# Optimization experiments

Measured on AMD Instinct MI355X. Metric: run time of the kernel, lower is better.

Reference implementation:

```python
import jax, jax.numpy as jnp
import numpy as np
from jax import lax

jax.config.update("jax_enable_x64", True)  # original torch code does the recurrence in float64

K_MAX = 32
L_MAX = 32
N = 65536


def setup_inputs() -> dict:
    key = jax.random.key(0)
    # strictly positive radii (r appears in a denominator)
    r = jax.random.uniform(key, (N,), dtype=jnp.float32, minval=0.1, maxval=10.0)
    return {"r": r}


def reference(r):
    # k = linspace(1, k_max, k_max)
    k = jnp.linspace(1.0, K_MAX, K_MAX, dtype=jnp.float64)          # [K]
    rk = r.astype(jnp.float64)[:, None] * k[None, :]                 # [N, K]

    lstart = L_MAX + int(np.sqrt(10 * L_MAX))                        # matches int(torch.sqrt(...))
    i_vals = jnp.arange(lstart, 0, -1, dtype=jnp.float64)            # lstart .. 1

    # downward (Miller) recurrence: j0 = (2i+1)/r * j1 - j2
    def step(carry, i):
        j1, j2 = carry
        j0 = (2.0 * i + 1.0) / rk * j1 - j2
        return (j0, j1), j0

    init = (jnp.ones_like(rk), jnp.zeros_like(rk))
    _, js = lax.scan(step, init, i_vals)                             # [lstart, N, K]

    # torch loop writes y[i-1] = j0 when i-1 < l_max, i.e. the last L_MAX
    # scan steps correspond to l = L_MAX-1 .. 0 -> reverse to get y[l]
    y = js[-L_MAX:][::-1]                                            # [L, N, K]

    # torch.sinc(x) = sin(pi x)/(pi x), so sinc(r/pi) = sin(r)/r = true j_0
    true_j0 = jnp.sinc(rk / jnp.pi)                                  # [N, K]
    y = y * true_j0 / y[0]                                           # normalize Miller recurrence

    # transpose(0,1): [L,N,K] -> [N,L,K], scale by sqrt(2/pi)*k
    out = jnp.transpose(y, (1, 0, 2)) * jnp.sqrt(2.0 / jnp.pi) * k[None, None, :]
    return out.astype(jnp.float32)
```

## Files before the change

kernel.cpp:

```cpp
#include <hip/hip_runtime.h>


#define K_MAX 32
#define L_MAX 32
#define LSTART 49

__global__ __launch_bounds__(256) void sph_bessel_kernel(
    const float* __restrict__ r, float* __restrict__ out, int n_total) {
    const int tid = blockIdx.x * blockDim.x + threadIdx.x;
    if (tid >= n_total * K_MAX) return;

    const int n  = tid >> 5;
    const int kq = tid & 31;
    const double kd = (double)(kq + 1);

    const double x   = (double)r[n] * kd;
    const double inv = 1.0 / x;

    double j1 = 1.0, j2 = 0.0;
#pragma unroll
    for (int i = LSTART; i >= 1; --i) {
        const double j0 = fma((2.0 * i + 1.0) * inv, j1, -j2);
        j2 = j1;
        j1 = j0;
    }
    const double y0 = j1;

    const double true_j0 = (double)sinf((float)x) * inv;
    const double scale   = (true_j0 / y0) * 0.79788456080286535588 * kd;

    float* op = out + (size_t)n * (L_MAX * K_MAX) + kq;
    j1 = 1.0;
    j2 = 0.0;
#pragma unroll
    for (int i = LSTART; i >= 1; --i) {
        const double j0 = fma((2.0 * i + 1.0) * inv, j1, -j2);
        j2 = j1;
        j1 = j0;
        if (i <= L_MAX) {
            op[(size_t)(i - 1) * K_MAX] = (float)(j0 * scale);
        }
    }
}

extern "C" void kernel_launch(void* const* d_in, const int* in_sizes, int n_in,
                              void* d_out, int out_size, void* d_ws, size_t ws_size,
                              hipStream_t stream) {
    const float* r = (const float*)d_in[0];
    float* out = (float*)d_out;
    const int n_total = in_sizes[0];

    const int total_threads = n_total * K_MAX;
    const int block = 256;
    const int grid = (total_threads + block - 1) / block;
    sph_bessel_kernel<<<grid, block, 0, stream>>>(r, out, n_total);
}
```

Before: 256.1 us.

## Compute four k values per thread with vectorized nontemporal float4 stores

Each thread now handles four consecutive k columns instead of one, so the thread count drops by four. The recurrences for the four columns are interleaved, which adds instruction-level parallelism. Output is written as 16-byte nontemporal vector stores instead of scalar 4-byte stores. The cost is more live double-precision registers per thread and fewer threads to hide latency.

New measurement: 271.9 us. 6.2% more time.

```diff
diff --git a/kernel.cpp b/kernel.cpp
--- a/kernel.cpp
+++ b/kernel.cpp
@@ -5,40 +5,68 @@
 #define L_MAX 32
 #define LSTART 49
 
+typedef float floatx4 __attribute__((ext_vector_type(4)));
+
 __global__ __launch_bounds__(256) void sph_bessel_kernel(
     const float* __restrict__ r, float* __restrict__ out, int n_total) {
     const int tid = blockIdx.x * blockDim.x + threadIdx.x;
-    if (tid >= n_total * K_MAX) return;
+    if (tid >= n_total * (K_MAX / 4)) return;
 
-    const int n  = tid >> 5;
-    const int kq = tid & 31;
-    const double kd = (double)(kq + 1);
+    const int n = tid >> 3;
+    const int q = tid & 7;
+    const double rd = (double)r[n];
 
-    const double x   = (double)r[n] * kd;
-    const double inv = 1.0 / x;
+    double inv[4], scale[4], j1[4], j2[4];
 
-    double j1 = 1.0, j2 = 0.0;
+#pragma unroll
+    for (int c = 0; c < 4; ++c) {
+        const double kd = (double)(4 * q + c + 1);
+        inv[c] = 1.0 / (rd * kd);
+        j1[c]  = 1.0;
+        j2[c]  = 0.0;
+    }
+
 #pragma unroll
     for (int i = LSTART; i >= 1; --i) {
-        const double j0 = fma((2.0 * i + 1.0) * inv, j1, -j2);
-        j2 = j1;
-        j1 = j0;
+        const double c2i = 2.0 * (double)i + 1.0;
+#pragma unroll
+        for (int c = 0; c < 4; ++c) {
+            const double j0 = fma(c2i * inv[c], j1[c], -j2[c]);
+            j2[c] = j1[c];
+            j1[c] = j0;
+        }
     }
-    const double y0 = j1;
 
-    const double true_j0 = (double)sinf((float)x) * inv;
-    const double scale   = (true_j0 / y0) * 0.79788456080286535588 * kd;
+#pragma unroll
+    for (int c = 0; c < 4; ++c) {
+        const double kd = (double)(4 * q + c + 1);
+        const double x  = rd * kd;
+        const double true_j0 = (double)sinf((float)x) * inv[c];
+        scale[c] = (true_j0 / j1[c]) * 0.79788456080286535588 * kd;
+        j1[c] = 1.0;
+        j2[c] = 0.0;
+    }
 
-    float* op = out + (size_t)n * (L_MAX * K_MAX) + kq;
-    j1 = 1.0;
-    j2 = 0.0;
+    float* op = out + (size_t)n * (L_MAX * K_MAX) + 4 * q;
 #pragma unroll
     for (int i = LSTART; i >= 1; --i) {
-        const double j0 = fma((2.0 * i + 1.0) * inv, j1, -j2);
-        j2 = j1;
-        j1 = j0;
+        const double c2i = 2.0 * (double)i + 1.0;
+        double j0c[4];
+#pragma unroll
+        for (int c = 0; c < 4; ++c) {
+            const double j0 = fma(c2i * inv[c], j1[c], -j2[c]);
+            j2[c] = j1[c];
+            j1[c] = j0;
+            j0c[c] = j0;
+        }
         if (i <= L_MAX) {
-            op[(size_t)(i - 1) * K_MAX] = (float)(j0 * scale);
+            floatx4 v;
+            v.x = (float)(j0c[0] * scale[0]);
+            v.y = (float)(j0c[1] * scale[1]);
+            v.z = (float)(j0c[2] * scale[2]);
+            v.w = (float)(j0c[3] * scale[3]);
+            __builtin_nontemporal_store(
+                v, (floatx4*)(op + (size_t)(i - 1) * K_MAX));
         }
     }
 }
@@ -50,7 +78,7 @@
     float* out = (float*)d_out;
     const int n_total = in_sizes[0];
 
-    const int total_threads = n_total * K_MAX;
+    const int total_threads = n_total * (K_MAX / 4);
     const int block = 256;
     const int grid = (total_threads + block - 1) / block;
     sph_bessel_kernel<<<grid, block, 0, stream>>>(r, out, n_total);
```
